# Kernel optimization log

Hardware: AMD Instinct MI355X
Metric: run time of the kernel (lower is better)

The kernel has to match this reference:

```python
import jax, jax.numpy as jnp
import numpy as np

N_EMBD = 1024
N_HEAD = 16
HEAD_DIM = N_EMBD // N_HEAD  # 64
N_CTX = 2048
ROPE_THETA = 10000.0


def _rope_cache(L, dim, base):
    inv_freq = 1.0 / (base ** (np.arange(0, dim, 2, dtype=np.float32) / dim))
    t = np.arange(L, dtype=np.float32)
    freqs = np.einsum('i,j->ij', t, inv_freq)  # (L, dim/2)
    return jnp.asarray(np.cos(freqs)), jnp.asarray(np.sin(freqs))


def _apply_rotary(x, cos, sin):
    # x: (B, H, L, D), cos/sin: (L, D/2) -> broadcast (1,1,L,D/2)
    x1 = x[..., ::2]
    x2 = x[..., 1::2]
    c = cos[None, None, :, :]
    s = sin[None, None, :, :]
    y1 = x1 * c - x2 * s
    y2 = x1 * s + x2 * c
    # interleave back: stack on last dim then flatten
    return jnp.stack((y1, y2), axis=-1).reshape(x.shape)


def setup_inputs() -> dict:
    key = jax.random.key(0)
    k1, k2, k3, k4, k5 = jax.random.split(key, 5)
    B, L, D = 4, 2048, N_EMBD
    scale = 0.02
    x = jax.random.normal(k1, (B, L, D), dtype=jnp.float32)
    W_qkv = jax.random.normal(k2, (D, 3 * D), dtype=jnp.float32) * scale
    b_qkv = jnp.zeros((3 * D,), dtype=jnp.float32)
    W_proj = jax.random.normal(k3, (D, D), dtype=jnp.float32) * scale
    b_proj = jnp.zeros((D,), dtype=jnp.float32)
    attention_mask = jnp.ones((B, L), dtype=jnp.int32)
    return {"x": x, "W_qkv": W_qkv, "b_qkv": b_qkv, "W_proj": W_proj,
            "b_proj": b_proj, "attention_mask": attention_mask}


def reference(x, W_qkv, b_qkv, W_proj, b_proj, attention_mask):
    B, L, D = x.shape
    H, Dh = N_HEAD, HEAD_DIM
    qkv = x @ W_qkv + b_qkv  # (B, L, 3D)
    q, k, v = jnp.split(qkv, 3, axis=2)
    # (B, L, H, Dh) -> (B, H, L, Dh)
    q = q.reshape(B, L, H, Dh).transpose(0, 2, 1, 3)
    k = k.reshape(B, L, H, Dh).transpose(0, 2, 1, 3)
    v = v.reshape(B, L, H, Dh).transpose(0, 2, 1, 3)
    cos, sin = _rope_cache(L, Dh, ROPE_THETA)
    q = _apply_rotary(q, cos, sin)
    k = _apply_rotary(k, cos, sin)
    # mask: causal & key padding keep
    causal = jnp.tril(jnp.ones((L, L), dtype=bool))[None, None]        # (1,1,L,L)
    key_keep = attention_mask.astype(bool)[:, None, None, :]          # (B,1,1,L)
    keep = causal & key_keep                                          # (B,1,L,L)
    scores = jnp.einsum('bhqd,bhkd->bhqk', q, k) / jnp.sqrt(jnp.float32(Dh))
    scores = jnp.where(keep, scores, jnp.finfo(scores.dtype).min)
    attn = jax.nn.softmax(scores, axis=-1)
    out = jnp.einsum('bhqk,bhkd->bhqd', attn, v)  # (B,H,L,Dh)
    out = out.transpose(0, 2, 1, 3).reshape(B, L, D)
    return out @ W_proj + b_proj
```

## Files before the change

### kernel.cpp

```cpp
#include <hip/hip_runtime.h>
#include <math.h>

typedef __bf16 bf16x8 __attribute__((ext_vector_type(8)));
typedef float f32x4 __attribute__((ext_vector_type(4)));
typedef float f32x16 __attribute__((ext_vector_type(16)));
typedef unsigned short u16;
typedef unsigned short u16x8 __attribute__((ext_vector_type(8)));
typedef unsigned short u16x4 __attribute__((ext_vector_type(4)));
typedef unsigned u32x2v __attribute__((ext_vector_type(2)));

#define BATCH 4
#define SEQ   2048
#define EMBD  1024
#define NHEAD 16
#define HDIM  64
#define MROWS 8192
#define QKVN  3072

__device__ __forceinline__ u16 f2bf(float f) {
    union { float f; unsigned u; } cv; cv.f = f;
    unsigned u = cv.u;
    return (u16)((u + 0x7FFFu + ((u >> 16) & 1u)) >> 16);
}

__device__ __forceinline__ unsigned cvtpk_bf16(float lo, float hi) {
    unsigned r;
    asm("v_cvt_pk_bf16_f32 %0, %1, %2" : "=v"(r) : "v"(lo), "v"(hi));
    return r;
}

__device__ __forceinline__ void glds16(const void* g, void* l) {
    __builtin_amdgcn_global_load_lds(
        (const __attribute__((address_space(1))) unsigned int*)(g),
        (__attribute__((address_space(3))) unsigned int*)(l), 16, 0, 0);
}

#define MF8(qm, A0, A1, A2, A3, B0, B1)                                          \
    acc[(qm)*4+0][0] = __builtin_amdgcn_mfma_f32_16x16x32_bf16(A0, B0, acc[(qm)*4+0][0], 0, 0, 0); \
    acc[(qm)*4+0][1] = __builtin_amdgcn_mfma_f32_16x16x32_bf16(A0, B1, acc[(qm)*4+0][1], 0, 0, 0); \
    acc[(qm)*4+1][0] = __builtin_amdgcn_mfma_f32_16x16x32_bf16(A1, B0, acc[(qm)*4+1][0], 0, 0, 0); \
    acc[(qm)*4+1][1] = __builtin_amdgcn_mfma_f32_16x16x32_bf16(A1, B1, acc[(qm)*4+1][1], 0, 0, 0); \
    acc[(qm)*4+2][0] = __builtin_amdgcn_mfma_f32_16x16x32_bf16(A2, B0, acc[(qm)*4+2][0], 0, 0, 0); \
    acc[(qm)*4+2][1] = __builtin_amdgcn_mfma_f32_16x16x32_bf16(A2, B1, acc[(qm)*4+2][1], 0, 0, 0); \
    acc[(qm)*4+3][0] = __builtin_amdgcn_mfma_f32_16x16x32_bf16(A3, B0, acc[(qm)*4+3][0], 0, 0, 0); \
    acc[(qm)*4+3][1] = __builtin_amdgcn_mfma_f32_16x16x32_bf16(A3, B1, acc[(qm)*4+3][1], 0, 0, 0);

__device__ __forceinline__ void transpose_body(const float* __restrict__ W,
                                               u16* __restrict__ Wt, int K, int N,
                                               int n0, int k0, u16 (*T)[68]) {
    const int tx = threadIdx.x & 15, ty = threadIdx.x >> 4;
#pragma unroll
    for (int r = 0; r < 4; r++) {
        int k = k0 + ty + r * 16;
        float4 w = *(const float4*)&W[(size_t)k * N + n0 + tx * 4];
        T[tx * 4 + 0][ty + r * 16] = f2bf(w.x);
        T[tx * 4 + 1][ty + r * 16] = f2bf(w.y);
        T[tx * 4 + 2][ty + r * 16] = f2bf(w.z);
        T[tx * 4 + 3][ty + r * 16] = f2bf(w.w);
    }
    __syncthreads();
#pragma unroll
    for (int r = 0; r < 4; r++) {
        int nl = ty + r * 16;
        u16x4 v = { T[nl][tx * 4 + 0], T[nl][tx * 4 + 1],
                    T[nl][tx * 4 + 2], T[nl][tx * 4 + 3] };
        *(u16x4*)&Wt[(size_t)(n0 + nl) * K + k0 + tx * 4] = v;
    }
}

__global__ __launch_bounds__(256)
void prep_kernel(const float* __restrict__ x, const float* __restrict__ Wqkv,
                 const float* __restrict__ Wproj, const int* __restrict__ amask,
                 u16* __restrict__ Xb, u16* __restrict__ Wqkvt, u16* __restrict__ Wprojt,
                 float* __restrict__ ropeC, float* __restrict__ ropeS,
                 float* __restrict__ mbias, int* __restrict__ flags) {
    __shared__ union { u16 T[64][68]; int ok[4]; } sm;
    const int bx = blockIdx.x, tid = threadIdx.x;
    if (bx < 8192) {
        int i = bx * 256 + tid;
        float4 v = ((const float4*)x)[i];
        u16x4 o = { f2bf(v.x), f2bf(v.y), f2bf(v.z), f2bf(v.w) };
        ((u16x4*)Xb)[i] = o;
    } else if (bx < 8960) {
        int bxx = bx - 8192;
        transpose_body(Wqkv, Wqkvt, EMBD, QKVN, (bxx % 48) * 64, (bxx / 48) * 64, sm.T);
    } else if (bx < 9216) {
        int bxx = bx - 8960;
        transpose_body(Wproj, Wprojt, EMBD, EMBD, (bxx & 15) * 64, (bxx >> 4) * 64, sm.T);
    } else if (bx < 9472) {
        int i = (bx - 9216) * 256 + tid;
        int l = i >> 5, p = i & 31;
        float invf = powf(10000.0f, -(float)(2 * p) * (1.0f / 64.0f));
        float sv, cv;
        sincosf((float)l * invf, &sv, &cv);
        ropeC[i] = cv; ropeS[i] = sv;
    } else {
        int idx = (bx - 9472) * 256 + tid;
        int mv = amask[idx];
        mbias[idx] = mv ? 0.0f : -1e30f;
        unsigned long long bal = __ballot(mv != 0);
        int wv = tid >> 6;
        if ((tid & 63) == 0) sm.ok[wv] = (bal == 0xFFFFFFFFFFFFFFFFull);
        __syncthreads();
        if (tid == 0)   flags[idx >> 7] = sm.ok[0] & sm.ok[1];
        if (tid == 128) flags[idx >> 7] = sm.ok[2] & sm.ok[3];
    }
}

__global__ __launch_bounds__(512, 2)
void qkv_gemm(const u16* __restrict__ A, const u16* __restrict__ Bt,
              const float* __restrict__ bias,
              const float* __restrict__ Ct, const float* __restrict__ St,
              u16* __restrict__ Qo, u16* __restrict__ Ko, u16* __restrict__ Vo) {
    __shared__ u16 SM[49152];
    const int tid = threadIdx.x;
    const int w = tid >> 6, ln = tid & 63;
    const int quad = ln >> 4, l16 = ln & 15;
    const int wm = w >> 2, wn = w & 3;
    const int bid = blockIdx.y * 24 + blockIdx.x;
    const int swz = (bid & 7) * 96 + (bid >> 3);
    const int m0 = (swz / 24) * 256, n0 = (swz % 24) * 128;

    const int sr8 = ln >> 3;
    const int xs = (ln & 7) ^ sr8;
    const u16* Ab = A  + (size_t)(m0 + w * 8 + sr8) * EMBD + xs * 8;
    const u16* Bb = Bt + (size_t)(n0 + w * 8 + sr8) * EMBD + xs * 8;
    u16* ldsA = SM + w * 512;
    u16* ldsB = SM + 32768 + w * 512;
    const int ch0 = ((0 + quad) ^ (l16 & 7)) * 8;
    const int ch1 = ((4 + quad) ^ (l16 & 7)) * 8;

    auto stageA = [&](int buf, int rb, int kt) {
        glds16(Ab + (size_t)rb * EMBD + kt * 64, ldsA + buf * 16384 + rb * 64);
    };
    auto stageB = [&](int buf, int rb, int kt) {
        glds16(Bb + (size_t)rb * EMBD + kt * 64, ldsB + buf * 8192 + rb * 64);
    };

    f32x4 acc[8][2] = {};

    stageA(0, 0, 0);  stageA(0, 128, 0);
    stageA(0, 64, 0); stageA(0, 192, 0);
    stageB(0, 0, 0);  stageB(0, 64, 0);
    stageA(1, 0, 1);  stageA(1, 128, 1);
    asm volatile("s_waitcnt vmcnt(2)" ::: "memory");
    __builtin_amdgcn_sched_barrier(0);
    __builtin_amdgcn_s_barrier();

    for (int u = 0; u < 16; ++u) {
        const int c = u & 1, nc = c ^ 1;
        const u16* Ac0 = SM + c * 16384 + (wm * 128 + l16) * 64;
        const u16* Ac1 = Ac0 + 64 * 64;
        const u16* Bc  = SM + 32768 + c * 8192 + (wn * 32 + l16) * 64;
        bf16x8 a0, a1, a2, a3, bk0a, bk0b, bk1a, bk1b;
        a0 = *(const bf16x8*)&Ac0[ch0];        a1 = *(const bf16x8*)&Ac0[1024 + ch0];
        a2 = *(const bf16x8*)&Ac0[2048 + ch0]; a3 = *(const bf16x8*)&Ac0[3072 + ch0];
        bk0a = *(const bf16x8*)&Bc[ch0];       bk0b = *(const bf16x8*)&Bc[1024 + ch0];
        if (u < 15) { stageA(nc, 64, u + 1); stageA(nc, 192, u + 1); stageB(nc, 64, u + 1); }
        __builtin_amdgcn_sched_barrier(0);
        __builtin_amdgcn_s_setprio(1);
        MF8(0, a0, a1, a2, a3, bk0a, bk0b);
        __builtin_amdgcn_s_setprio(0);
        __builtin_amdgcn_sched_barrier(0);
        a0 = *(const bf16x8*)&Ac0[ch1];        a1 = *(const bf16x8*)&Ac0[1024 + ch1];
        a2 = *(const bf16x8*)&Ac0[2048 + ch1]; a3 = *(const bf16x8*)&Ac0[3072 + ch1];
        bk1a = *(const bf16x8*)&Bc[ch1];       bk1b = *(const bf16x8*)&Bc[1024 + ch1];
        if (u < 15) stageB(nc, 0, u + 1);
        __builtin_amdgcn_sched_barrier(0);
        __builtin_amdgcn_s_setprio(1);
        MF8(0, a0, a1, a2, a3, bk1a, bk1b);
        __builtin_amdgcn_s_setprio(0);
        __builtin_amdgcn_sched_barrier(0);
        __builtin_amdgcn_s_barrier();
        a0 = *(const bf16x8*)&Ac1[ch0];        a1 = *(const bf16x8*)&Ac1[1024 + ch0];
        a2 = *(const bf16x8*)&Ac1[2048 + ch0]; a3 = *(const bf16x8*)&Ac1[3072 + ch0];
        if (u < 14) { stageA(c, 0, u + 2); stageA(c, 128, u + 2); }
        __builtin_amdgcn_sched_barrier(0);
        __builtin_amdgcn_s_setprio(1);
        MF8(1, a0, a1, a2, a3, bk0a, bk0b);
        __builtin_amdgcn_s_setprio(0);
        __builtin_amdgcn_sched_barrier(0);
        a0 = *(const bf16x8*)&Ac1[ch1];        a1 = *(const bf16x8*)&Ac1[1024 + ch1];
        a2 = *(const bf16x8*)&Ac1[2048 + ch1]; a3 = *(const bf16x8*)&Ac1[3072 + ch1];
        __builtin_amdgcn_sched_barrier(0);
        __builtin_amdgcn_s_setprio(1);
        MF8(1, a0, a1, a2, a3, bk1a, bk1b);
        __builtin_amdgcn_s_setprio(0);
        __builtin_amdgcn_sched_barrier(0);
        if (u < 14) asm volatile("s_waitcnt vmcnt(2)" ::: "memory");
        else        asm volatile("s_waitcnt vmcnt(0)" ::: "memory");
        __builtin_amdgcn_sched_barrier(0);
        __builtin_amdgcn_s_barrier();
    }

    const int sec = n0 >> 10;
    if (sec == 2) {
#pragma unroll
        for (int ii = 0; ii < 8; ii++)
#pragma unroll
            for (int r = 0; r < 4; r++) {
                int m = m0 + wm * 128 + ii * 16 + quad * 4 + r;
                int b = m >> 11, l = m & 2047;
#pragma unroll
                for (int j = 0; j < 2; j++) {
                    int n = n0 + wn * 32 + j * 16 + l16;
                    int dcol = n & 1023;
                    int h = dcol >> 6, dh = dcol & 63;
                    float v = acc[ii][j][r] + bias[n];
                    Vo[(((size_t)b * NHEAD + h) * SEQ + l) * HDIM + dh] = f2bf(v);
                }
            }
    } else {
        u16* O = (sec == 0) ? Qo : Ko;
        const float qs = (sec == 0) ? 0.125f * 1.44269504f : 1.0f;
#pragma unroll
        for (int ii = 0; ii < 8; ii++)
#pragma unroll
            for (int r = 0; r < 4; r++) {
                int m = m0 + wm * 128 + ii * 16 + quad * 4 + r;
                int b = m >> 11, l = m & 2047;
#pragma unroll
                for (int j = 0; j < 2; j++) {
                    int n = n0 + wn * 32 + j * 16 + l16;
                    int h = (n & 1023) >> 6, dh = n & 63;
                    int p = (n & 63) >> 1;
                    float v = acc[ii][j][r] + bias[n];
                    float pv = __shfl_xor(v, 1, 64);
                    float cv = Ct[l * 32 + p], sv = St[l * 32 + p];
                    float o = (l16 & 1) ? (pv * sv + v * cv) : (v * cv - pv * sv);
                    O[(((size_t)b * NHEAD + h) * SEQ + l) * HDIM + dh] = f2bf(o * qs);
                }
            }
    }
}

__global__ __launch_bounds__(256)
void transpose_v(const u16* __restrict__ Vo, u16* __restrict__ Vt) {
    __shared__ u16 T[64][72];
    const int bh = blockIdx.y;
    const int l0 = blockIdx.x * 64;
    const int tx = threadIdx.x & 15, ty = threadIdx.x >> 4;
#pragma unroll
    for (int rr = 0; rr < 4; rr++) {
        int l = ty + rr * 16;
        u16x4 v = *(const u16x4*)&Vo[((size_t)bh * SEQ + l0 + l) * HDIM + tx * 4];
        T[l][tx * 4 + 0] = v.x; T[l][tx * 4 + 1] = v.y;
        T[l][tx * 4 + 2] = v.z; T[l][tx * 4 + 3] = v.w;
    }
    __syncthreads();
#pragma unroll
    for (int rr = 0; rr < 4; rr++) {
        int dh = ty + rr * 16;
        u16x4 w = { T[tx * 4 + 0][dh], T[tx * 4 + 1][dh],
                    T[tx * 4 + 2][dh], T[tx * 4 + 3][dh] };
        *(u16x4*)&Vt[((size_t)bh * HDIM + dh) * SEQ + l0 + tx * 4] = w;
    }
}

__global__ __launch_bounds__(256)
void attn_mfma3(const u16* __restrict__ Qb, const u16* __restrict__ Kb,
                const u16* __restrict__ Vt, const float* __restrict__ mb,
                const int* __restrict__ flags, u16* __restrict__ Ot) {
    __shared__ u16 SM[32768];
    const int tid = threadIdx.x;
    const int wv = tid >> 6, ln = tid & 63;
    const int l32 = ln & 31, hi = ln >> 5;
    const int bh = blockIdx.x & 63;
    const int pr = blockIdx.x >> 6;
    const int b = bh >> 4;
    const u16* Qg = Qb + (size_t)bh * SEQ * HDIM;
    const u16* Kg = Kb + (size_t)bh * SEQ * HDIM;
    const u16* Vg = Vt + (size_t)bh * HDIM * SEQ;

    const int kRow = ln >> 3;
    const size_t kLane = (size_t)(wv * 32 + kRow) * 64 + ((ln & 7) ^ kRow) * 8;
    const int vRow = ln >> 4, sc0 = (ln & 15) ^ vRow;
    const size_t vLaneE = (size_t)(wv * 16 + vRow) * SEQ + sc0 * 8;
    const size_t vLaneO = (size_t)(wv * 16 + vRow) * SEQ + (sc0 ^ 4) * 8;

    for (int pass = 0; pass < 2; pass++) {
        const int qt = pass ? pr : 15 - pr;
        const int q0w = qt * 128 + wv * 32;

        bf16x8 Qf[4];
#pragma unroll
        for (int kd = 0; kd < 4; kd++)
            Qf[kd] = *(const bf16x8*)&Qg[(size_t)(q0w + l32) * HDIM + kd * 16 + hi * 8];

        f32x16 o[2] = {};
        float mrun = -1e30f, lrun = 0.f;

        {
            u16* KsD = SM + wv * 2048;
            u16* VsD = SM + 8192 + wv * 2048;
#pragma unroll
            for (int p = 0; p < 4; p++) {
                glds16(Kg + kLane + p * 512, KsD + p * 512);
                glds16(Vg + ((p & 1) ? vLaneO : vLaneE) + (size_t)p * 4 * SEQ, VsD + p * 512);
            }
        }
        __syncthreads();

        int buf = 0;
        for (int kt = 0; kt <= qt; kt++) {
            const int kbase = kt * 128;
            if (kt < qt) {
                const size_t nb = (size_t)(kbase + 128);
                u16* KsD = SM + (buf ^ 1) * 16384 + wv * 2048;
                u16* VsD = SM + (buf ^ 1) * 16384 + 8192 + wv * 2048;
#pragma unroll
                for (int p = 0; p < 4; p++) {
                    glds16(Kg + nb * 64 + kLane + p * 512, KsD + p * 512);
                    glds16(Vg + nb + ((p & 1) ? vLaneO : vLaneE) + (size_t)p * 4 * SEQ, VsD + p * 512);
                }
            }
            const u16* Ks = SM + buf * 16384;
            const u16* Vs = SM + buf * 16384 + 8192;

            f32x16 s[4];
            __builtin_amdgcn_s_setprio(1);
#pragma unroll
            for (int mi = 0; mi < 4; mi++) {
                const int key = mi * 32 + l32;
                f32x16 z = {};
#pragma unroll
                for (int kd = 0; kd < 4; kd++) {
                    int ch = kd * 2 + hi;
                    bf16x8 kf = *(const bf16x8*)&Ks[key * 64 + ((ch ^ (key & 7)) * 8)];
                    z = __builtin_amdgcn_mfma_f32_32x32x16_bf16(kf, Qf[kd], z, 0, 0, 0);
                }
                s[mi] = z;
            }
            __builtin_amdgcn_s_setprio(0);

            if (kt == qt) {
                const int qloc = wv * 32 + l32;
#pragma unroll
                for (int mi = 0; mi < 4; mi++)
#pragma unroll
                    for (int r = 0; r < 16; r++) {
                        int row = mi * 32 + (r & 3) + 8 * (r >> 2) + 4 * hi;
                        if (row > qloc) s[mi][r] = -1e30f;
                    }
            }
            if (!flags[b * 16 + kt]) {
#pragma unroll
                for (int mi = 0; mi < 4; mi++)
#pragma unroll
                    for (int r = 0; r < 16; r++) {
                        int row = mi * 32 + (r & 3) + 8 * (r >> 2) + 4 * hi;
                        s[mi][r] += mb[b * SEQ + kbase + row];
                    }
            }

            float rm = -1e30f;
#pragma unroll
            for (int mi = 0; mi < 4; mi++) {
                float a0 = fmaxf(fmaxf(s[mi][0],  s[mi][1]),  fmaxf(s[mi][2],  s[mi][3]));
                float a1 = fmaxf(fmaxf(s[mi][4],  s[mi][5]),  fmaxf(s[mi][6],  s[mi][7]));
                float a2 = fmaxf(fmaxf(s[mi][8],  s[mi][9]),  fmaxf(s[mi][10], s[mi][11]));
                float a3 = fmaxf(fmaxf(s[mi][12], s[mi][13]), fmaxf(s[mi][14], s[mi][15]));
                rm = fmaxf(rm, fmaxf(fmaxf(a0, a1), fmaxf(a2, a3)));
            }
            {
                u32x2v f = __builtin_amdgcn_permlane32_swap(
                    __float_as_uint(rm), __float_as_uint(rm), false, false);
                rm = fmaxf(__uint_as_float(f[0]), __uint_as_float(f[1]));
            }
            if (!__all(rm <= mrun + 8.0f)) {
                float mnew = fmaxf(mrun, rm);
                float al = __builtin_amdgcn_exp2f(mrun - mnew);
                mrun = mnew;
                lrun *= al;
#pragma unroll
                for (int r = 0; r < 16; r++) { o[0][r] *= al; o[1][r] *= al; }
            }
            float rs = 0.f;
#pragma unroll
            for (int mi = 0; mi < 4; mi++) {
                float ps = 0.f;
#pragma unroll
                for (int r = 0; r < 16; r++) {
                    float pe = __builtin_amdgcn_exp2f(s[mi][r] - mrun);
                    s[mi][r] = pe;
                    ps += pe;
                }
                rs += ps;
            }
            {
                u32x2v f = __builtin_amdgcn_permlane32_swap(
                    __float_as_uint(rs), __float_as_uint(rs), false, false);
                rs = __uint_as_float(f[0]) + __uint_as_float(f[1]);
            }
            lrun += rs;

#pragma unroll
            for (int t = 0; t < 4; t++) {
                unsigned A0 = cvtpk_bf16(s[t][0],  s[t][1]);
                unsigned B0 = cvtpk_bf16(s[t][4],  s[t][5]);
                unsigned A1 = cvtpk_bf16(s[t][2],  s[t][3]);
                unsigned B1 = cvtpk_bf16(s[t][6],  s[t][7]);
                u32x2v r0 = __builtin_amdgcn_permlane32_swap(A0, B0, false, false);
                u32x2v r1 = __builtin_amdgcn_permlane32_swap(A1, B1, false, false);
                union { unsigned u[4]; bf16x8 v; } p0;
                p0.u[0] = r0[0]; p0.u[1] = r1[0]; p0.u[2] = r0[1]; p0.u[3] = r1[1];

                unsigned A2 = cvtpk_bf16(s[t][8],  s[t][9]);
                unsigned B2 = cvtpk_bf16(s[t][12], s[t][13]);
                unsigned A3 = cvtpk_bf16(s[t][10], s[t][11]);
                unsigned B3 = cvtpk_bf16(s[t][14], s[t][15]);
                u32x2v r2 = __builtin_amdgcn_permlane32_swap(A2, B2, false, false);
                u32x2v r3 = __builtin_amdgcn_permlane32_swap(A3, B3, false, false);
                union { unsigned u[4]; bf16x8 v; } p1;
                p1.u[0] = r2[0]; p1.u[1] = r3[0]; p1.u[2] = r2[1]; p1.u[3] = r3[1];

                __builtin_amdgcn_s_setprio(1);
#pragma unroll
                for (int md = 0; md < 2; md++) {
                    const int dh = md * 32 + l32;
                    bf16x8 v0 = *(const bf16x8*)&Vs[dh * 128 + (((t * 4 + hi)     ^ (dh & 7)) * 8)];
                    o[md] = __builtin_amdgcn_mfma_f32_32x32x16_bf16(v0, p0.v, o[md], 0, 0, 0);
                    bf16x8 v1 = *(const bf16x8*)&Vs[dh * 128 + (((t * 4 + 2 + hi) ^ (dh & 7)) * 8)];
                    o[md] = __builtin_amdgcn_mfma_f32_32x32x16_bf16(v1, p1.v, o[md], 0, 0, 0);
                }
                __builtin_amdgcn_s_setprio(0);
            }
            __syncthreads();
            buf ^= 1;
        }

        u16* Osh = SM + wv * 2176;
        float inv = 1.0f / lrun;
#pragma unroll
        for (int md = 0; md < 2; md++)
#pragma unroll
            for (int r = 0; r < 16; r++) {
                int dh = md * 32 + (r & 3) + 8 * (r >> 2) + 4 * hi;
                Osh[l32 * 68 + dh] = f2bf(o[md][r] * inv);
            }
        __syncthreads();
        {
            int qrow = ln >> 1, hf = ln & 1;
            size_t gbase = ((size_t)bh * SEQ + qt * 128 + wv * 32 + qrow) * HDIM + hf * 32;
#pragma unroll
            for (int c = 0; c < 4; c++) {
                u16x8 vv = *(const u16x8*)&Osh[qrow * 68 + hf * 32 + c * 8];
                *(u16x8*)&Ot[gbase + c * 8] = vv;
            }
        }
        __syncthreads();
    }
}

__global__ __launch_bounds__(512, 2)
void proj_gemm(const u16* __restrict__ A, const u16* __restrict__ Bt,
               const float* __restrict__ bias, float* __restrict__ out) {
    __shared__ u16 SM[49152];
    const int tid = threadIdx.x;
    const int w = tid >> 6, ln = tid & 63;
    const int quad = ln >> 4, l16 = ln & 15;
    const int wm = w >> 2, wn = w & 3;
    const int bid = blockIdx.y * 8 + blockIdx.x;
    const int swz = (bid & 7) * 32 + (bid >> 3);
    const int m0 = (swz >> 3) * 256, n0 = (swz & 7) * 128;

    const int sr8 = ln >> 3;
    const int xs = (ln & 7) ^ sr8;
    const int aRow = m0 + w * 8 + sr8;
    const int bb16 = (aRow >> 11) * 16;
    const int lrow = aRow & 2047;
    const u16* Ap = A + ((size_t)bb16 * SEQ + lrow) * HDIM + xs * 8;
    const u16* Bb = Bt + (size_t)(n0 + w * 8 + sr8) * EMBD + xs * 8;
    u16* ldsA = SM + w * 512;
    u16* ldsB = SM + 32768 + w * 512;
    const int ch0 = ((0 + quad) ^ (l16 & 7)) * 8;
    const int ch1 = ((4 + quad) ^ (l16 & 7)) * 8;

    auto stageA = [&](int buf, int rb, int kt) {
        glds16(Ap + ((size_t)kt * SEQ + rb) * HDIM, ldsA + buf * 16384 + rb * 64);
    };
    auto stageB = [&](int buf, int rb, int kt) {
        glds16(Bb + (size_t)rb * EMBD + kt * 64, ldsB + buf * 8192 + rb * 64);
    };

    f32x4 acc[8][2] = {};

    stageA(0, 0, 0);  stageA(0, 128, 0);
    stageA(0, 64, 0); stageA(0, 192, 0);
    stageB(0, 0, 0);  stageB(0, 64, 0);
    stageA(1, 0, 1);  stageA(1, 128, 1);
    asm volatile("s_waitcnt vmcnt(2)" ::: "memory");
    __builtin_amdgcn_sched_barrier(0);
    __builtin_amdgcn_s_barrier();

    for (int u = 0; u < 16; ++u) {
        const int c = u & 1, nc = c ^ 1;
        const u16* Ac0 = SM + c * 16384 + (wm * 128 + l16) * 64;
        const u16* Ac1 = Ac0 + 64 * 64;
        const u16* Bc  = SM + 32768 + c * 8192 + (wn * 32 + l16) * 64;
        bf16x8 a0, a1, a2, a3, bk0a, bk0b, bk1a, bk1b;
        a0 = *(const bf16x8*)&Ac0[ch0];        a1 = *(const bf16x8*)&Ac0[1024 + ch0];
        a2 = *(const bf16x8*)&Ac0[2048 + ch0]; a3 = *(const bf16x8*)&Ac0[3072 + ch0];
        bk0a = *(const bf16x8*)&Bc[ch0];       bk0b = *(const bf16x8*)&Bc[1024 + ch0];
        if (u < 15) { stageA(nc, 64, u + 1); stageA(nc, 192, u + 1); stageB(nc, 64, u + 1); }
        __builtin_amdgcn_sched_barrier(0);
        __builtin_amdgcn_s_setprio(1);
        MF8(0, a0, a1, a2, a3, bk0a, bk0b);
        __builtin_amdgcn_s_setprio(0);
        __builtin_amdgcn_sched_barrier(0);
        a0 = *(const bf16x8*)&Ac0[ch1];        a1 = *(const bf16x8*)&Ac0[1024 + ch1];
        a2 = *(const bf16x8*)&Ac0[2048 + ch1]; a3 = *(const bf16x8*)&Ac0[3072 + ch1];
        bk1a = *(const bf16x8*)&Bc[ch1];       bk1b = *(const bf16x8*)&Bc[1024 + ch1];
        if (u < 15) stageB(nc, 0, u + 1);
        __builtin_amdgcn_sched_barrier(0);
        __builtin_amdgcn_s_setprio(1);
        MF8(0, a0, a1, a2, a3, bk1a, bk1b);
        __builtin_amdgcn_s_setprio(0);
        __builtin_amdgcn_sched_barrier(0);
        __builtin_amdgcn_s_barrier();
        a0 = *(const bf16x8*)&Ac1[ch0];        a1 = *(const bf16x8*)&Ac1[1024 + ch0];
        a2 = *(const bf16x8*)&Ac1[2048 + ch0]; a3 = *(const bf16x8*)&Ac1[3072 + ch0];
        if (u < 14) { stageA(c, 0, u + 2); stageA(c, 128, u + 2); }
        __builtin_amdgcn_sched_barrier(0);
        __builtin_amdgcn_s_setprio(1);
        MF8(1, a0, a1, a2, a3, bk0a, bk0b);
        __builtin_amdgcn_s_setprio(0);
        __builtin_amdgcn_sched_barrier(0);
        a0 = *(const bf16x8*)&Ac1[ch1];        a1 = *(const bf16x8*)&Ac1[1024 + ch1];
        a2 = *(const bf16x8*)&Ac1[2048 + ch1]; a3 = *(const bf16x8*)&Ac1[3072 + ch1];
        __builtin_amdgcn_sched_barrier(0);
        __builtin_amdgcn_s_setprio(1);
        MF8(1, a0, a1, a2, a3, bk1a, bk1b);
        __builtin_amdgcn_s_setprio(0);
        __builtin_amdgcn_sched_barrier(0);
        if (u < 14) asm volatile("s_waitcnt vmcnt(2)" ::: "memory");
        else        asm volatile("s_waitcnt vmcnt(0)" ::: "memory");
        __builtin_amdgcn_sched_barrier(0);
        __builtin_amdgcn_s_barrier();
    }

#pragma unroll
    for (int ii = 0; ii < 8; ii++)
#pragma unroll
        for (int r = 0; r < 4; r++) {
            int m = m0 + wm * 128 + ii * 16 + quad * 4 + r;
#pragma unroll
            for (int j = 0; j < 2; j++) {
                int n = n0 + wn * 32 + j * 16 + l16;
                out[(size_t)m * EMBD + n] = acc[ii][j][r] + bias[n];
            }
        }
}

extern "C" void kernel_launch(void* const* d_in, const int* in_sizes, int n_in,
                              void* d_out, int out_size, void* d_ws, size_t ws_size,
                              hipStream_t stream)
{
    const float* x     = (const float*)d_in[0];
    const float* Wqkv  = (const float*)d_in[1];
    const float* bqkv  = (const float*)d_in[2];
    const float* Wproj = (const float*)d_in[3];
    const float* bproj = (const float*)d_in[4];
    const int*   amask = (const int*)d_in[5];
    float* out = (float*)d_out;

    char* ws = (char*)d_ws;
    u16*   Xb     = (u16*)(ws);
    u16*   Ot     = (u16*)(ws);
    u16*   Wqkvt  = (u16*)(ws + 16777216);
    u16*   Wprojt = (u16*)(ws + 23068672);
    u16*   Qb     = (u16*)(ws + 25165824);
    u16*   Kb     = (u16*)(ws + 41943040);
    u16*   Vb     = (u16*)(ws + 58720256);
    u16*   Vtp    = (u16*)(ws + 75497472);
    float* ropeC  = (float*)(ws + 92274688);
    float* ropeS  = (float*)(ws + 92536832);
    float* mbias  = (float*)(ws + 92798976);
    int*   flags  = (int*)(ws + 92831744);

    prep_kernel<<<9504, 256, 0, stream>>>(x, Wqkv, Wproj, amask,
                                          Xb, Wqkvt, Wprojt, ropeC, ropeS, mbias, flags);
    qkv_gemm<<<dim3(24, 32), 512, 0, stream>>>(
        Xb, Wqkvt, bqkv, ropeC, ropeS, Qb, Kb, Vb);
    transpose_v<<<dim3(32, 64), 256, 0, stream>>>(Vb, Vtp);
    attn_mfma3<<<512, 256, 0, stream>>>(Qb, Kb, Vtp, mbias, flags, Ot);
    proj_gemm<<<dim3(8, 32), 512, 0, stream>>>(Ot, Wprojt, bproj, out);
}
```

Before: 255.8 us.

## Fold softmax max-subtraction into MFMA init, flip pass order, simplify proj GEMM

The attention kernel now seeds the QK MFMA accumulator with the negated running max, so scores arrive already shifted and only a rescale branch subtracts the new tile max. Row max and sum reductions are vectorised, and odd blocks reverse their pass order to balance causal work. The projection GEMM is replaced with a simpler 128x128-tile, 256-thread double-buffered kernel in place of the hand-scheduled 256x128 one. The GEMM change trades the old fine-grained load/MFMA interleaving for simpler code and more blocks.

```diff
diff --git a/kernel.cpp b/kernel.cpp
--- a/kernel.cpp
+++ b/kernel.cpp
@@ -2,7 +2,9 @@
 #include <math.h>
 
 typedef __bf16 bf16x8 __attribute__((ext_vector_type(8)));
+typedef float f32x2 __attribute__((ext_vector_type(2)));
 typedef float f32x4 __attribute__((ext_vector_type(4)));
+typedef float f32x8 __attribute__((ext_vector_type(8)));
 typedef float f32x16 __attribute__((ext_vector_type(16)));
 typedef unsigned short u16;
 typedef unsigned short u16x8 __attribute__((ext_vector_type(8)));
@@ -33,6 +35,29 @@
     __builtin_amdgcn_global_load_lds(
         (const __attribute__((address_space(1))) unsigned int*)(g),
         (__attribute__((address_space(3))) unsigned int*)(l), 16, 0, 0);
+}
+
+__device__ __forceinline__ float hmax16(f32x16 v) {
+    f32x8 a = __builtin_elementwise_max(
+        __builtin_shufflevector(v, v, 0, 1, 2, 3, 4, 5, 6, 7),
+        __builtin_shufflevector(v, v, 8, 9, 10, 11, 12, 13, 14, 15));
+    f32x4 b = __builtin_elementwise_max(
+        __builtin_shufflevector(a, a, 0, 1, 2, 3),
+        __builtin_shufflevector(a, a, 4, 5, 6, 7));
+    f32x2 c = __builtin_elementwise_max(
+        __builtin_shufflevector(b, b, 0, 1),
+        __builtin_shufflevector(b, b, 2, 3));
+    return fmaxf(c[0], c[1]);
+}
+
+__device__ __forceinline__ float hsum16(f32x16 v) {
+    f32x8 a = __builtin_shufflevector(v, v, 0, 1, 2, 3, 4, 5, 6, 7)
+            + __builtin_shufflevector(v, v, 8, 9, 10, 11, 12, 13, 14, 15);
+    f32x4 b = __builtin_shufflevector(a, a, 0, 1, 2, 3)
+            + __builtin_shufflevector(a, a, 4, 5, 6, 7);
+    f32x2 c = __builtin_shufflevector(b, b, 0, 1)
+            + __builtin_shufflevector(b, b, 2, 3);
+    return c[0] + c[1];
 }
 
 #define MF8(qm, A0, A1, A2, A3, B0, B1)                                          \
@@ -267,6 +292,7 @@
     const int l32 = ln & 31, hi = ln >> 5;
     const int bh = blockIdx.x & 63;
     const int pr = blockIdx.x >> 6;
+    const int flip = blockIdx.x & 1;
     const int b = bh >> 4;
     const u16* Qg = Qb + (size_t)bh * SEQ * HDIM;
     const u16* Kg = Kb + (size_t)bh * SEQ * HDIM;
@@ -279,7 +305,7 @@
     const size_t vLaneO = (size_t)(wv * 16 + vRow) * SEQ + (sc0 ^ 4) * 8;
 
     for (int pass = 0; pass < 2; pass++) {
-        const int qt = pass ? pr : 15 - pr;
+        const int qt = (pass ^ flip) ? pr : 15 - pr;
         const int q0w = qt * 128 + wv * 32;
 
         bf16x8 Qf[4];
@@ -288,7 +314,8 @@
             Qf[kd] = *(const bf16x8*)&Qg[(size_t)(q0w + l32) * HDIM + kd * 16 + hi * 8];
 
         f32x16 o[2] = {};
-        float mrun = -1e30f, lrun = 0.f;
+        f32x16 zin = {};
+        float mrun = 0.0f, lrun = 0.f;
 
         {
             u16* KsD = SM + wv * 2048;
@@ -322,7 +349,7 @@
 #pragma unroll
             for (int mi = 0; mi < 4; mi++) {
                 const int key = mi * 32 + l32;
-                f32x16 z = {};
+                f32x16 z = zin;
 #pragma unroll
                 for (int kd = 0; kd < 4; kd++) {
                     int ch = kd * 2 + hi;
@@ -353,40 +380,34 @@
                     }
             }
 
-            float rm = -1e30f;
-#pragma unroll
-            for (int mi = 0; mi < 4; mi++) {
-                float a0 = fmaxf(fmaxf(s[mi][0],  s[mi][1]),  fmaxf(s[mi][2],  s[mi][3]));
-                float a1 = fmaxf(fmaxf(s[mi][4],  s[mi][5]),  fmaxf(s[mi][6],  s[mi][7]));
-                float a2 = fmaxf(fmaxf(s[mi][8],  s[mi][9]),  fmaxf(s[mi][10], s[mi][11]));
-                float a3 = fmaxf(fmaxf(s[mi][12], s[mi][13]), fmaxf(s[mi][14], s[mi][15]));
-                rm = fmaxf(rm, fmaxf(fmaxf(a0, a1), fmaxf(a2, a3)));
-            }
+            float rm = hmax16(__builtin_elementwise_max(
+                __builtin_elementwise_max(s[0], s[1]),
+                __builtin_elementwise_max(s[2], s[3])));
             {
                 u32x2v f = __builtin_amdgcn_permlane32_swap(
                     __float_as_uint(rm), __float_as_uint(rm), false, false);
                 rm = fmaxf(__uint_as_float(f[0]), __uint_as_float(f[1]));
             }
-            if (!__all(rm <= mrun + 8.0f)) {
-                float mnew = fmaxf(mrun, rm);
-                float al = __builtin_amdgcn_exp2f(mrun - mnew);
-                mrun = mnew;
+            if (!__all(rm <= 8.0f)) {
+                float al = __builtin_amdgcn_exp2f(-rm);
+                mrun += rm;
                 lrun *= al;
-#pragma unroll
-                for (int r = 0; r < 16; r++) { o[0][r] *= al; o[1][r] *= al; }
-            }
-            float rs = 0.f;
-#pragma unroll
-            for (int mi = 0; mi < 4; mi++) {
-                float ps = 0.f;
-#pragma unroll
-                for (int r = 0; r < 16; r++) {
-                    float pe = __builtin_amdgcn_exp2f(s[mi][r] - mrun);
-                    s[mi][r] = pe;
-                    ps += pe;
-                }
-                rs += ps;
-            }
+                o[0] *= al; o[1] *= al;
+#pragma unroll
+                for (int r = 0; r < 16; r++) zin[r] = -mrun;
+#pragma unroll
+                for (int mi = 0; mi < 4; mi++)
+#pragma unroll
+                    for (int r = 0; r < 16; r++)
+                        s[mi][r] = __builtin_amdgcn_exp2f(s[mi][r] - rm);
+            } else {
+#pragma unroll
+                for (int mi = 0; mi < 4; mi++)
+#pragma unroll
+                    for (int r = 0; r < 16; r++)
+                        s[mi][r] = __builtin_amdgcn_exp2f(s[mi][r]);
+            }
+            float rs = hsum16((s[0] + s[1]) + (s[2] + s[3]));
             {
                 u32x2v f = __builtin_amdgcn_permlane32_swap(
                     __float_as_uint(rs), __float_as_uint(rs), false, false);
@@ -452,102 +473,78 @@
     }
 }
 
-__global__ __launch_bounds__(512, 2)
+__global__ __launch_bounds__(256)
 void proj_gemm(const u16* __restrict__ A, const u16* __restrict__ Bt,
                const float* __restrict__ bias, float* __restrict__ out) {
-    __shared__ u16 SM[49152];
+    __shared__ u16 SM[32768];
     const int tid = threadIdx.x;
-    const int w = tid >> 6, ln = tid & 63;
+    const int wv = tid >> 6, ln = tid & 63;
     const int quad = ln >> 4, l16 = ln & 15;
-    const int wm = w >> 2, wn = w & 3;
     const int bid = blockIdx.y * 8 + blockIdx.x;
-    const int swz = (bid & 7) * 32 + (bid >> 3);
-    const int m0 = (swz >> 3) * 256, n0 = (swz & 7) * 128;
-
-    const int sr8 = ln >> 3;
-    const int xs = (ln & 7) ^ sr8;
-    const int aRow = m0 + w * 8 + sr8;
-    const int bb16 = (aRow >> 11) * 16;
-    const int lrow = aRow & 2047;
-    const u16* Ap = A + ((size_t)bb16 * SEQ + lrow) * HDIM + xs * 8;
-    const u16* Bb = Bt + (size_t)(n0 + w * 8 + sr8) * EMBD + xs * 8;
-    u16* ldsA = SM + w * 512;
-    u16* ldsB = SM + 32768 + w * 512;
-    const int ch0 = ((0 + quad) ^ (l16 & 7)) * 8;
-    const int ch1 = ((4 + quad) ^ (l16 & 7)) * 8;
-
-    auto stageA = [&](int buf, int rb, int kt) {
-        glds16(Ap + ((size_t)kt * SEQ + rb) * HDIM, ldsA + buf * 16384 + rb * 64);
+    const int swz = (bid & 7) * 64 + (bid >> 3);
+    const int m0 = (swz >> 3) * 128, n0 = (swz & 7) * 128;
+    const int wm = wv >> 1, wn = wv & 1;
+
+    const int srow = wv * 8 + (ln >> 3);
+    const int xs = (ln & 7) ^ (srow & 7);
+
+    f32x4 acc[4][4] = {};
+
+    auto stage = [&](int buf, int kt) {
+        u16* As = SM + buf * 16384;
+        u16* Bs = As + 8192;
+#pragma unroll
+        for (int p = 0; p < 4; p++) {
+            int row = p * 32 + srow;
+            int m = m0 + row;
+            int bb = m >> 11, l = m & 2047;
+            glds16(A + (((size_t)(bb * 16 + kt) * SEQ + l) * HDIM) + xs * 8,
+                   As + (p * 256 + wv * 64) * 8);
+            glds16(Bt + (size_t)(n0 + row) * EMBD + kt * 64 + xs * 8,
+                   Bs + (p * 256 + wv * 64) * 8);
+        }
     };
-    auto stageB = [&](int buf, int rb, int kt) {
-        glds16(Bb + (size_t)rb * EMBD + kt * 64, ldsB + buf * 8192 + rb * 64);
-    };
-
-    f32x4 acc[8][2] = {};
-
-    stageA(0, 0, 0);  stageA(0, 128, 0);
-    stageA(0, 64, 0); stageA(0, 192, 0);
-    stageB(0, 0, 0);  stageB(0, 64, 0);
-    stageA(1, 0, 1);  stageA(1, 128, 1);
-    asm volatile("s_waitcnt vmcnt(2)" ::: "memory");
-    __builtin_amdgcn_sched_barrier(0);
-    __builtin_amdgcn_s_barrier();
-
-    for (int u = 0; u < 16; ++u) {
-        const int c = u & 1, nc = c ^ 1;
-        const u16* Ac0 = SM + c * 16384 + (wm * 128 + l16) * 64;
-        const u16* Ac1 = Ac0 + 64 * 64;
-        const u16* Bc  = SM + 32768 + c * 8192 + (wn * 32 + l16) * 64;
-        bf16x8 a0, a1, a2, a3, bk0a, bk0b, bk1a, bk1b;
-        a0 = *(const bf16x8*)&Ac0[ch0];        a1 = *(const bf16x8*)&Ac0[1024 + ch0];
-        a2 = *(const bf16x8*)&Ac0[2048 + ch0]; a3 = *(const bf16x8*)&Ac0[3072 + ch0];
-        bk0a = *(const bf16x8*)&Bc[ch0];       bk0b = *(const bf16x8*)&Bc[1024 + ch0];
-        if (u < 15) { stageA(nc, 64, u + 1); stageA(nc, 192, u + 1); stageB(nc, 64, u + 1); }
-        __builtin_amdgcn_sched_barrier(0);
+
+    stage(0, 0);
+    __syncthreads();
+    int buf = 0;
+    for (int kt = 0; kt < 16; kt++) {
+        if (kt < 15) stage(buf ^ 1, kt + 1);
+        const u16* As = SM + buf * 16384;
+        const u16* Bs = As + 8192;
         __builtin_amdgcn_s_setprio(1);
-        MF8(0, a0, a1, a2, a3, bk0a, bk0b);
+#pragma unroll
+        for (int kk = 0; kk < 2; kk++) {
+            bf16x8 af[4], bfr[4];
+#pragma unroll
+            for (int i = 0; i < 4; i++) {
+                int R = wm * 64 + i * 16 + l16;
+                af[i] = *(const bf16x8*)&As[R * 64 + (((kk * 4 + quad) ^ (R & 7)) * 8)];
+            }
+#pragma unroll
+            for (int j = 0; j < 4; j++) {
+                int R = wn * 64 + j * 16 + l16;
+                bfr[j] = *(const bf16x8*)&Bs[R * 64 + (((kk * 4 + quad) ^ (R & 7)) * 8)];
+            }
+#pragma unroll
+            for (int i = 0; i < 4; i++)
+#pragma unroll
+                for (int j = 0; j < 4; j++)
+                    acc[i][j] = __builtin_amdgcn_mfma_f32_16x16x32_bf16(af[i], bfr[j], acc[i][j], 0, 0, 0);
+        }
         __builtin_amdgcn_s_setprio(0);
-        __builtin_amdgcn_sched_barrier(0);
-        a0 = *(const bf16x8*)&Ac0[ch1];        a1 = *(const bf16x8*)&Ac0[1024 + ch1];
-        a2 = *(const bf16x8*)&Ac0[2048 + ch1]; a3 = *(const bf16x8*)&Ac0[3072 + ch1];
-        bk1a = *(const bf16x8*)&Bc[ch1];       bk1b = *(const bf16x8*)&Bc[1024 + ch1];
-        if (u < 15) stageB(nc, 0, u + 1);
-        __builtin_amdgcn_sched_barrier(0);
-        __builtin_amdgcn_s_setprio(1);
-        MF8(0, a0, a1, a2, a3, bk1a, bk1b);
-        __builtin_amdgcn_s_setprio(0);
-        __builtin_amdgcn_sched_barrier(0);
-        __builtin_amdgcn_s_barrier();
-        a0 = *(const bf16x8*)&Ac1[ch0];        a1 = *(const bf16x8*)&Ac1[1024 + ch0];
-        a2 = *(const bf16x8*)&Ac1[2048 + ch0]; a3 = *(const bf16x8*)&Ac1[3072 + ch0];
-        if (u < 14) { stageA(c, 0, u + 2); stageA(c, 128, u + 2); }
-        __builtin_amdgcn_sched_barrier(0);
-        __builtin_amdgcn_s_setprio(1);
-        MF8(1, a0, a1, a2, a3, bk0a, bk0b);
-        __builtin_amdgcn_s_setprio(0);
-        __builtin_amdgcn_sched_barrier(0);
-        a0 = *(const bf16x8*)&Ac1[ch1];        a1 = *(const bf16x8*)&Ac1[1024 + ch1];
-        a2 = *(const bf16x8*)&Ac1[2048 + ch1]; a3 = *(const bf16x8*)&Ac1[3072 + ch1];
-        __builtin_amdgcn_sched_barrier(0);
-        __builtin_amdgcn_s_setprio(1);
-        MF8(1, a0, a1, a2, a3, bk1a, bk1b);
-        __builtin_amdgcn_s_setprio(0);
-        __builtin_amdgcn_sched_barrier(0);
-        if (u < 14) asm volatile("s_waitcnt vmcnt(2)" ::: "memory");
-        else        asm volatile("s_waitcnt vmcnt(0)" ::: "memory");
-        __builtin_amdgcn_sched_barrier(0);
-        __builtin_amdgcn_s_barrier();
-    }
-
-#pragma unroll
-    for (int ii = 0; ii < 8; ii++)
+        __syncthreads();
+        buf ^= 1;
+    }
+#pragma unroll
+    for (int i = 0; i < 4; i++)
 #pragma unroll
         for (int r = 0; r < 4; r++) {
-            int m = m0 + wm * 128 + ii * 16 + quad * 4 + r;
-#pragma unroll
-            for (int j = 0; j < 2; j++) {
-                int n = n0 + wn * 32 + j * 16 + l16;
-                out[(size_t)m * EMBD + n] = acc[ii][j][r] + bias[n];
+            int m = m0 + wm * 64 + i * 16 + quad * 4 + r;
+#pragma unroll
+            for (int j = 0; j < 4; j++) {
+                int n = n0 + wn * 64 + j * 16 + l16;
+                out[(size_t)m * EMBD + n] = acc[i][j][r] + bias[n];
             }
         }
 }
@@ -584,5 +581,5 @@
         Xb, Wqkvt, bqkv, ropeC, ropeS, Qb, Kb, Vb);
     transpose_v<<<dim3(32, 64), 256, 0, stream>>>(Vb, Vtp);
     attn_mfma3<<<512, 256, 0, stream>>>(Qb, Kb, Vtp, mbias, flags, Ot);
-    proj_gemm<<<dim3(8, 32), 512, 0, stream>>>(Ot, Wprojt, bproj, out);
-}
+    proj_gemm<<<dim3(EMBD / 128, MROWS / 128), 256, 0, stream>>>(Ot, Wprojt, bproj, out);
+}
```

New measurement: 279.7 us. 1.09x slower.
